# Kernel optimization log

Hardware: AMD Instinct MI355X
Metric: run time of the kernel (lower is better)

Reference implementation:

```python
import jax, jax.numpy as jnp
import numpy as np

B, S, D, H, F = 4, 1024, 512, 8, 2048
EPS = 1e-6


def _layernorm(x, g, b):
    m = jnp.mean(x, axis=-1, keepdims=True)
    v = jnp.mean(jnp.square(x - m), axis=-1, keepdims=True)
    return (x - m) * jax.lax.rsqrt(v + EPS) * g + b


def setup_inputs() -> dict:
    key = jax.random.key(0)
    ks = jax.random.split(key, 16)
    sd = 0.02
    return {
        "input_tensor": jax.random.normal(ks[0], (B, S, D), jnp.float32),
        # per-head QKV projections: each head maps D -> D (full depth, as in source)
        "Wq": jax.random.normal(ks[1], (H, D, D), jnp.float32) * sd,
        "bq": jnp.zeros((H, D), jnp.float32),
        "Wk": jax.random.normal(ks[2], (H, D, D), jnp.float32) * sd,
        "bk": jnp.zeros((H, D), jnp.float32),
        "Wv": jax.random.normal(ks[3], (H, D, D), jnp.float32) * sd,
        "bv": jnp.zeros((H, D), jnp.float32),
        # output projection after concat of H full-depth heads: (H*D) -> D
        "Wo": jax.random.normal(ks[4], (H * D, D), jnp.float32) * sd,
        "bo": jnp.zeros((D,), jnp.float32),
        "g1": jnp.ones((D,), jnp.float32),
        "beta1": jnp.zeros((D,), jnp.float32),
        "W1": jax.random.normal(ks[5], (D, F), jnp.float32) * sd,
        "b1": jnp.zeros((F,), jnp.float32),
        "W2": jax.random.normal(ks[6], (F, D), jnp.float32) * sd,
        "b2": jnp.zeros((D,), jnp.float32),
        "g2": jnp.ones((D,), jnp.float32),
        "beta2": jnp.zeros((D,), jnp.float32),
    }


def reference(input_tensor, Wq, bq, Wk, bk, Wv, bv, Wo, bo,
              g1, beta1, W1, b1, W2, b2, g2, beta2):
    x = input_tensor
    # batched per-head projections: [B,S,D] x [H,D,E] -> [B,H,S,E]
    q = jnp.einsum("bsd,hde->bhse", x, Wq) + bq[None, :, None, :]
    k = jnp.einsum("bsd,hde->bhse", x, Wk) + bk[None, :, None, :]
    v = jnp.einsum("bsd,hde->bhse", x, Wv) + bv[None, :, None, :]
    scale = 1.0 / jnp.sqrt(jnp.asarray(D, x.dtype))
    scores = jnp.einsum("bhse,bhte->bhst", q, k) * scale  # [B,H,S,S]
    attn = jax.nn.softmax(scores, axis=-1)
    heads = jnp.einsum("bhst,bhte->bhse", attn, v)  # [B,H,S,E]
    # concat heads on last axis: [B,S,H*D]
    concat = jnp.transpose(heads, (0, 2, 1, 3)).reshape(B, S, H * D)
    mha = concat @ Wo + bo  # [B,S,D]
    # dropout is identity at inference
    y = _layernorm(x + mha, g1, beta1)
    ff = jax.nn.relu(y @ W1 + b1) @ W2 + b2
    return _layernorm(y + ff, g2, beta2)
```

## Files before the change

### kernel.cpp

```cpp
#include <hip/hip_runtime.h>
#include <hip/hip_bf16.h>

typedef unsigned short u16;
typedef unsigned char u8;
typedef unsigned int u32;
typedef long long i64;
typedef __attribute__((ext_vector_type(4))) float f32x4;
typedef __attribute__((ext_vector_type(8))) __bf16 bf16x8;

#define DEV __device__ __forceinline__

DEV u16 f2bf(float f) {
  union { float f; unsigned u; } c; c.f = f;
  unsigned r = (c.u + 0x7fffu + ((c.u >> 16) & 1u)) >> 16;
  return (u16)r;
}

DEV float bf2f(u16 u) {
  union { u32 u; float f; } c; c.u = (u32)u << 16;
  return c.f;
}

DEV void gld_lds16(const void* g, void* l) {
  __builtin_amdgcn_global_load_lds(
      (__attribute__((address_space(1))) void*)g,
      (__attribute__((address_space(3))) void*)l, 16, 0, 0);
}

DEV f32x4 mfma_bf16(bf16x8 a, bf16x8 b, f32x4 c) {
  return __builtin_amdgcn_mfma_f32_16x16x32_bf16(a, b, c, 0, 0, 0);
}

DEV void bar_vm0() { asm volatile("s_waitcnt vmcnt(0) lgkmcnt(0)\n\ts_barrier" ::: "memory"); }
DEV void wait_lg0() { asm volatile("s_waitcnt lgkmcnt(0)" ::: "memory"); }

DEV u32 pack_fp8x4(float a, float b, float c, float d) {
  u32 t = __builtin_amdgcn_cvt_pk_fp8_f32(a, b, 0, false);
  t = __builtin_amdgcn_cvt_pk_fp8_f32(c, d, t, true);
  return t;
}

DEV u8 f2fp8(float v) {
  u32 t = __builtin_amdgcn_cvt_pk_fp8_f32(v, v, 0, false);
  return (u8)(t & 0xff);
}

__global__ __launch_bounds__(256) void prep_kernel(const float* __restrict__ x,
                                                   const float* __restrict__ Wq,
                                                   const float* __restrict__ Wk,
                                                   const float* __restrict__ Wv,
                                                   const float* __restrict__ Wo,
                                                   const float* __restrict__ W1,
                                                   const float* __restrict__ W2,
                                                   u16* __restrict__ xb, u16* __restrict__ wqC,
                                                   u16* __restrict__ wkC, u16* __restrict__ wvC,
                                                   u16* __restrict__ woT, u16* __restrict__ w1T,
                                                   u16* __restrict__ w2T) {
  int b = blockIdx.x;
  int tid = threadIdx.x;
  if (b < 8192) {
    const float* in;
    u16* out;
    int i;
    if (b < 2048) { in = x; out = xb; i = b * 256 + tid; }
    else {
      int idx = b - 2048;
      int job = idx >> 11;
      in = job == 0 ? Wq : (job == 1 ? Wk : Wv);
      out = job == 0 ? wqC : (job == 1 ? wkC : wvC);
      i = (idx & 2047) * 256 + tid;
    }
    float4 v = ((const float4*)in)[i];
    ushort4 o;
    o.x = f2bf(v.x); o.y = f2bf(v.y); o.z = f2bf(v.z); o.w = f2bf(v.w);
    ((ushort4*)out)[i] = o;
    return;
  }
  int idx = b - 8192;
  const float* in;
  u16* out;
  int R, C, bx, by;
  if (idx < 2048) { in = Wo; out = woT; R = 4096; C = 512; by = idx >> 4; bx = idx & 15; }
  else if (idx < 3072) { int rr = idx - 2048; in = W1; out = w1T; R = 512; C = 2048; by = rr >> 6; bx = rr & 63; }
  else { int rr = idx - 3072; in = W2; out = w2T; R = 2048; C = 512; by = rr >> 4; bx = rr & 15; }
  __shared__ float t[32][33];
  int c0 = bx * 32, r0 = by * 32;
  int tx = tid & 31, ty = tid >> 5;
#pragma unroll
  for (int i = 0; i < 4; ++i) {
    int rr2 = ty + i * 8;
    t[rr2][tx] = in[(size_t)(r0 + rr2) * C + c0 + tx];
  }
  __syncthreads();
#pragma unroll
  for (int i = 0; i < 4; ++i) {
    int cc = ty + i * 8;
    out[(size_t)(c0 + cc) * R + r0 + tx] = f2bf(t[tx][cc]);
  }
}

__global__ __launch_bounds__(256) void biasp_kernel(const float* __restrict__ Wo,
                                                    const float* __restrict__ bv,
                                                    float* __restrict__ biasP) {
  int b = blockIdx.x;
  int h = b >> 2, ec = b & 3;
  int t = threadIdx.x;
  int tl = t & 127, half = t >> 7;
  int e = ec * 128 + tl;
  float acc = 0.f;
  for (int i = 0; i < 256; ++i) {
    int e2 = half * 256 + i;
    acc += Wo[(size_t)(h * 512 + e2) * 512 + e] * bv[h * 512 + e2];
  }
  __shared__ float sh[2][128];
  sh[half][tl] = acc;
  __syncthreads();
  if (half == 0) biasP[h * 512 + e] = sh[0][tl] + sh[1][tl];
}

template <int AMODE>
__global__ __launch_bounds__(256) void gemm_bat(const u16* __restrict__ A,
                                                const u16* __restrict__ B,
                                                u16* __restrict__ out) {
  constexpr int BK = 64, BM = 128, BN = 128;
  __shared__ u16 As[2][BM * BK];
  __shared__ u16 Bs[2][BN * BK];
  const int tid = threadIdx.x;
  const int wave = tid >> 6, lane = tid & 63;
  const int r = lane & 15, g = lane >> 4;
  const int row0 = blockIdx.y * BM, col0 = blockIdx.x * BN;
  const int head = row0 >> 9;
  const int wr = (wave >> 1) * 64, wc = (wave & 1) * 64;

  auto stage = [&](int kt, int p) {
#pragma unroll
    for (int i = 0; i < 4; ++i) {
      int bi = i * 256 + wave * 64;
      int c = bi + lane;
      int row = c >> 3, ch = (c & 7) ^ (row & 7);
      size_t aoff;
      if constexpr (AMODE == 0)
        aoff = (size_t)(row0 + row) * 512 + kt + ch * 8;
      else
        aoff = (size_t)((row0 + row) & 511) * 4096 + head * 512 + kt + ch * 8;
      gld_lds16(A + aoff, &As[p][(size_t)bi * 8]);
    }
#pragma unroll
    for (int i = 0; i < 4; ++i) {
      int bi = i * 256 + wave * 64;
      int c = bi + lane;
      int row = c >> 3, ch = (c & 7) ^ (row & 7);
      gld_lds16(B + (size_t)(head * 512 + col0 + row) * 512 + kt + ch * 8,
                &Bs[p][(size_t)bi * 8]);
    }
  };

  f32x4 acc[4][4] = {};
  stage(0, 0);
  for (int t = 0; t < 8; ++t) {
    const int p = t & 1;
    bar_vm0();
    if (t < 7) stage((t + 1) * BK, p ^ 1);
    __builtin_amdgcn_s_setprio(1);
#pragma unroll
    for (int kk = 0; kk < 2; ++kk) {
      bf16x8 af[4], bfv[4];
#pragma unroll
      for (int m = 0; m < 4; ++m)
        af[m] = *(const bf16x8*)(&As[p][(wr + m * 16 + r) * BK + (((kk * 4 + g) ^ (r & 7))) * 8]);
#pragma unroll
      for (int n = 0; n < 4; ++n)
        bfv[n] = *(const bf16x8*)(&Bs[p][(wc + n * 16 + r) * BK + (((kk * 4 + g) ^ (r & 7))) * 8]);
#pragma unroll
      for (int m = 0; m < 4; ++m)
#pragma unroll
        for (int n = 0; n < 4; ++n)
          acc[m][n] = mfma_bf16(af[m], bfv[n], acc[m][n]);
    }
    __builtin_amdgcn_s_setprio(0);
  }
#pragma unroll
  for (int m = 0; m < 4; ++m)
#pragma unroll
    for (int n = 0; n < 4; ++n)
#pragma unroll
      for (int j = 0; j < 4; ++j)
        out[(size_t)(row0 + wr + m * 16 + g * 4 + j) * 512 + col0 + wc + n * 16 + r] =
            f2bf(acc[m][n][j]);
}

template <int NT, int BM, int BN, int WM, int WN, int MODE, int SPLITK>
__global__ __launch_bounds__(NT) void gemm_tn(const u16* __restrict__ A,
                                              const u16* __restrict__ B, int N, int K,
                                              void* __restrict__ out0,
                                              const float* __restrict__ bias0) {
  constexpr int BK = 64;
  constexpr int MF = WM / 16, NF = WN / 16;
  constexpr int WC = BN / WN;
  constexpr int AI = (BM * BK / 8) / NT;
  constexpr int BI = (BN * BK / 8) / NT;
  __shared__ u16 As[2][BM * BK];
  __shared__ u16 Bs[2][BN * BK];
  const int tid = threadIdx.x;
  const int wave = tid >> 6, lane = tid & 63;
  const int r = lane & 15, g = lane >> 4;
  const int row0 = blockIdx.y * BM, col0 = blockIdx.x * BN;
  const int wr = (wave / WC) * WM, wc = (wave % WC) * WN;
  const int KS = K * SPLITK;
  const int kb0 = blockIdx.z * K;

  auto stage = [&](int kt, int p) {
#pragma unroll
    for (int i = 0; i < AI; ++i) {
      int bi = i * NT + wave * 64;
      int c = bi + lane;
      int row = c >> 3, ch = (c & 7) ^ (row & 7);
      gld_lds16(A + (size_t)(row0 + row) * KS + kb0 + kt + ch * 8, &As[p][(size_t)bi * 8]);
    }
#pragma unroll
    for (int i = 0; i < BI; ++i) {
      int bi = i * NT + wave * 64;
      int c = bi + lane;
      int row = c >> 3, ch = (c & 7) ^ (row & 7);
      gld_lds16(B + (size_t)(col0 + row) * KS + kb0 + kt + ch * 8, &Bs[p][(size_t)bi * 8]);
    }
  };

  f32x4 acc[MF][NF] = {};
  const int nt = K / BK;

  stage(0, 0);
  for (int t = 0; t < nt; ++t) {
    const int p = t & 1;
    bar_vm0();
    if (t + 1 < nt) stage((t + 1) * BK, p ^ 1);
    __builtin_amdgcn_s_setprio(1);
#pragma unroll
    for (int kk = 0; kk < 2; ++kk) {
      bf16x8 af[MF], bfv[NF];
#pragma unroll
      for (int m = 0; m < MF; ++m)
        af[m] = *(const bf16x8*)(&As[p][(wr + m * 16 + r) * BK + (((kk * 4 + g) ^ (r & 7))) * 8]);
#pragma unroll
      for (int n = 0; n < NF; ++n)
        bfv[n] = *(const bf16x8*)(&Bs[p][(wc + n * 16 + r) * BK + (((kk * 4 + g) ^ (r & 7))) * 8]);
#pragma unroll
      for (int m = 0; m < MF; ++m)
#pragma unroll
        for (int n = 0; n < NF; ++n)
          acc[m][n] = mfma_bf16(af[m], bfv[n], acc[m][n]);
    }
    __builtin_amdgcn_s_setprio(0);
  }

  const size_t moff = (size_t)blockIdx.z * gridDim.y * BM * N;
#pragma unroll
  for (int m = 0; m < MF; ++m) {
#pragma unroll
    for (int n = 0; n < NF; ++n) {
      int gcol = col0 + wc + n * 16 + r;
#pragma unroll
      for (int j = 0; j < 4; ++j) {
        int grow = row0 + wr + m * 16 + g * 4 + j;
        float val = acc[m][n][j];
        if constexpr (MODE == 0) {
          int he = gcol;
          val += bias0[he];
          int bb = grow >> 10, s = grow & 1023;
          size_t off = (((size_t)(bb * 8 + (he >> 9)) * 1024 + s) * 512) + (he & 511);
          ((u16*)out0)[off] = f2bf(val);
        } else if constexpr (MODE == 1) {
          val += bias0[grow];
          int bb = gcol >> 10, s = gcol & 1023;
          size_t off = (((size_t)bb * 8 + (grow >> 9)) * 512 + (grow & 511)) * 1024 + s;
          ((u8*)out0)[off] = f2fp8(val);
        } else if constexpr (MODE == 2) {
          if (SPLITK == 1 || blockIdx.z == 0) val += bias0[gcol];
          ((float*)out0)[moff + (size_t)grow * N + gcol] = val;
        } else {
          float v2 = fmaxf(val + bias0[gcol], 0.0f);
          ((u16*)out0)[(size_t)grow * N + gcol] = f2bf(v2);
        }
      }
    }
  }
}

__global__ __launch_bounds__(512, 2) void flash_kernel(const u16* __restrict__ qg,
                                                       const u16* __restrict__ kg,
                                                       const u8* __restrict__ vtg,
                                                       u16* __restrict__ concat) {
  constexpr float SCALE = 0.04419417382415922f;
  __shared__ u16 Ks[2][32 * 512];
  __shared__ __align__(16) u8 VsB[2][16 * 1024];
  __shared__ __align__(16) u32 PsP[8][128];

  const int tid = threadIdx.x;
  const int wave = tid >> 6, lane = tid & 63;
  const int r = lane & 15, g = lane >> 4;
  const int bx = blockIdx.x;
  const int xcd = bx & 7, slot = bx >> 3;
  const int bh = xcd * 4 + (slot >> 3);
  const int qt = slot & 7;
  const int bb = bh >> 3, hh = bh & 7;
  const size_t hbase = (size_t)bh * 1024 * 512;
  const u16* qp = qg + hbase;
  const u16* kp = kg + (size_t)bb * 1024 * 512;
  const u8* vp = vtg + (size_t)bh * 512 * 1024;
  const int q0 = qt * 128;

  bf16x8 q[16];
#pragma unroll
  for (int kk = 0; kk < 16; ++kk)
    q[kk] = *(const bf16x8*)(qp + (size_t)(q0 + wave * 16 + r) * 512 + kk * 32 + g * 8);

  const int krow8 = lane >> 3, kch = (lane & 7) ^ (lane >> 3);
  const int vrow_s = lane >> 1;
  const int vsw_s = (vrow_s & 2) ^ ((vrow_s >> 2) & 2);
  const int vhalf = lane & 1;
  auto stageKV = [&](int t, int p) {
    int kv = t * 32;
#pragma unroll
    for (int j = 0; j < 4; ++j) {
      int id = wave * 4 + j;
      gld_lds16(kp + (size_t)(kv + j * 8 + krow8) * 512 + wave * 64 + kch * 8,
                &Ks[p][id * 512]);
    }
#pragma unroll
    for (int jj = 0; jj < 2; ++jj) {
      int nv = wave * 2 + jj;
      gld_lds16(vp + (size_t)(nv * 32 + vrow_s) * 1024 + kv + (((vhalf * 2) ^ vsw_s) * 8),
                &VsB[p][nv * 1024]);
    }
  };

  f32x4 o[32] = {};
  float mrun = -1e30f, lrun = 0.f;

  stageKV(0, 0);

  const int krh = (r >> 3) * 512;
  const int ke0 = (r & 7) * 64 + ((g ^ (r & 7)) * 8);
  const int ke1 = (r & 7) * 64 + (((4 + g) ^ (r & 7)) * 8);
  const int vsw = (r & 2) ^ ((r >> 2) & 2);
  const int vo8 = ((g ^ vsw) << 3);
  const int psw = r & 6;

  for (int t = 0; t < 32; ++t) {
    const int p = t & 1;
    bar_vm0();
    if (t < 31) stageKV(t + 1, p ^ 1);

    __builtin_amdgcn_s_setprio(1);
    f32x4 a0 = {}, a1 = {}, b0 = {}, b1 = {};
#pragma unroll
    for (int kc = 0; kc < 8; ++kc) {
      const u16* kb = &Ks[p][kc * 2048 + krh];
      bf16x8 kf00 = *(const bf16x8*)(kb + ke0);
      bf16x8 kf01 = *(const bf16x8*)(kb + 1024 + ke0);
      bf16x8 kf10 = *(const bf16x8*)(kb + ke1);
      bf16x8 kf11 = *(const bf16x8*)(kb + 1024 + ke1);
      a0 = mfma_bf16(kf00, q[2 * kc], a0);
      b0 = mfma_bf16(kf01, q[2 * kc], b0);
      a1 = mfma_bf16(kf10, q[2 * kc + 1], a1);
      b1 = mfma_bf16(kf11, q[2 * kc + 1], b1);
    }
    __builtin_amdgcn_s_setprio(0);
    f32x4 s0 = a0 + a1;
    f32x4 s1 = b0 + b1;

    float m8 = -1e30f;
#pragma unroll
    for (int j = 0; j < 4; ++j) {
      s0[j] *= SCALE;
      s1[j] *= SCALE;
      m8 = fmaxf(m8, fmaxf(s0[j], s1[j]));
    }
    m8 = fmaxf(m8, __shfl_xor(m8, 16));
    m8 = fmaxf(m8, __shfl_xor(m8, 32));
    if (__any(m8 - mrun > 6.0f)) {
      float mn = fmaxf(mrun, m8);
      float rs = __expf(mrun - mn);
      mrun = mn;
      lrun *= rs;
#pragma unroll
      for (int j = 0; j < 4; ++j) {
        float rsj = __shfl(rs, (lane & 48) | (g * 4 + j));
#pragma unroll
        for (int n = 0; n < 32; ++n) o[n][j] *= rsj;
      }
    }
    f32x4 p0, p1;
    float ls = 0.f;
#pragma unroll
    for (int j = 0; j < 4; ++j) {
      p0[j] = __expf(s0[j] - mrun);
      p1[j] = __expf(s1[j] - mrun);
      ls += p0[j] + p1[j];
    }
    ls += __shfl_xor(ls, 16);
    ls += __shfl_xor(ls, 32);
    lrun += ls;

    {
      u32* pw = PsP[wave];
      u32 wA = pack_fp8x4(p0[0], p0[1], p0[2], p0[3]);
      u32 wB = pack_fp8x4(p1[0], p1[1], p1[2], p1[3]);
      pw[r * 8 + (g ^ psw)] = wA;
      pw[r * 8 + ((4 + g) ^ psw)] = wB;
    }
    wait_lg0();

    i64 pa = *(const i64*)&PsP[wave][r * 8 + ((2 * g) ^ psw)];
    __builtin_amdgcn_s_setprio(1);
#pragma unroll
    for (int n = 0; n < 32; ++n) {
      int vrow = ((n & 1) << 4) + r;
      i64 bv = *(const i64*)&VsB[p][((n >> 1) << 10) + vrow * 32 + vo8];
      o[n] = __builtin_amdgcn_mfma_f32_16x16x32_fp8_fp8(pa, bv, o[n], 0, 0, 0);
    }
    __builtin_amdgcn_s_setprio(0);
  }

  float invl = 1.0f / lrun;
#pragma unroll
  for (int j = 0; j < 4; ++j) {
    float inv = __shfl(invl, (lane & 48) | (g * 4 + j));
    int srow = q0 + wave * 16 + g * 4 + j;
    size_t rowoff = ((size_t)bb * 1024 + srow) * 4096;
#pragma unroll
    for (int n = 0; n < 32; ++n) {
      int ocol = hh * 512 + n * 16 + r;
      concat[rowoff + ocol] = f2bf(o[n][j] * inv);
    }
  }
}

__global__ __launch_bounds__(128) void add_ln_kernel(const float* __restrict__ xin,
                                                     const u16* __restrict__ cc8,
                                                     const float* __restrict__ addin,
                                                     const float* __restrict__ addin2,
                                                     const float* __restrict__ bias,
                                                     const float* __restrict__ gamma,
                                                     const float* __restrict__ beta,
                                                     float* __restrict__ yout,
                                                     u16* __restrict__ ybout) {
  int row = blockIdx.x;
  int t = threadIdx.x;
  float4 xv = ((const float4*)(xin + (size_t)row * 512))[t];
  float v0 = xv.x, v1 = xv.y, v2 = xv.z, v3 = xv.w;
  if (cc8) {
    const u16* cr = cc8 + (size_t)row * 4096 + t * 4;
#pragma unroll
    for (int h = 0; h < 8; ++h) {
      ushort4 u = *(const ushort4*)(cr + h * 512);
      v0 += bf2f(u.x); v1 += bf2f(u.y); v2 += bf2f(u.z); v3 += bf2f(u.w);
    }
  }
  if (addin) {
    float4 av = ((const float4*)(addin + (size_t)row * 512))[t];
    v0 += av.x; v1 += av.y; v2 += av.z; v3 += av.w;
  }
  if (addin2) {
    float4 bv2 = ((const float4*)(addin2 + (size_t)row * 512))[t];
    v0 += bv2.x; v1 += bv2.y; v2 += bv2.z; v3 += bv2.w;
  }
  if (bias) {
    float4 b4 = ((const float4*)bias)[t];
    v0 += b4.x; v1 += b4.y; v2 += b4.z; v3 += b4.w;
  }
  float s1 = v0 + v1 + v2 + v3;
  float s2 = v0 * v0 + v1 * v1 + v2 * v2 + v3 * v3;
#pragma unroll
  for (int d = 1; d < 64; d <<= 1) {
    s1 += __shfl_xor(s1, d);
    s2 += __shfl_xor(s2, d);
  }
  __shared__ float sh[4];
  int wv = t >> 6;
  if ((t & 63) == 0) { sh[wv * 2] = s1; sh[wv * 2 + 1] = s2; }
  __syncthreads();
  s1 = sh[0] + sh[2];
  s2 = sh[1] + sh[3];
  float mean = s1 * (1.0f / 512.0f);
  float var = s2 * (1.0f / 512.0f) - mean * mean;
  float rstd = rsqrtf(var + 1e-6f);
  float4 gv = ((const float4*)gamma)[t];
  float4 bv = ((const float4*)beta)[t];
  float o0 = (v0 - mean) * rstd * gv.x + bv.x;
  float o1 = (v1 - mean) * rstd * gv.y + bv.y;
  float o2 = (v2 - mean) * rstd * gv.z + bv.z;
  float o3 = (v3 - mean) * rstd * gv.w + bv.w;
  float4 ov; ov.x = o0; ov.y = o1; ov.z = o2; ov.w = o3;
  ((float4*)(yout + (size_t)row * 512))[t] = ov;
  if (ybout) {
    ushort4 ub;
    ub.x = f2bf(o0); ub.y = f2bf(o1); ub.z = f2bf(o2); ub.w = f2bf(o3);
    ((ushort4*)(ybout + (size_t)row * 512))[t] = ub;
  }
}

extern "C" void kernel_launch(void* const* d_in, const int* in_sizes, int n_in, void* d_out,
                              int out_size, void* d_ws, size_t ws_size, hipStream_t stream) {
  (void)in_sizes; (void)n_in; (void)out_size; (void)ws_size;
  const float* x   = (const float*)d_in[0];
  const float* Wq  = (const float*)d_in[1];
  const float* bq  = (const float*)d_in[2];
  const float* Wk  = (const float*)d_in[3];
  const float* bk  = (const float*)d_in[4];
  const float* Wv  = (const float*)d_in[5];
  const float* bv  = (const float*)d_in[6];
  const float* Wo  = (const float*)d_in[7];
  const float* bo  = (const float*)d_in[8];
  const float* g1  = (const float*)d_in[9];
  const float* be1 = (const float*)d_in[10];
  const float* W1  = (const float*)d_in[11];
  const float* b1  = (const float*)d_in[12];
  const float* W2  = (const float*)d_in[13];
  const float* b2  = (const float*)d_in[14];
  const float* g2  = (const float*)d_in[15];
  const float* be2 = (const float*)d_in[16];
  (void)bk;

  char* ws = (char*)d_ws;
  const size_t MB = 1024 * 1024;
  u16*   xb    = (u16*)(ws + 0);
  u16*   wqC   = (u16*)(ws + 4 * MB);
  u16*   wkC   = (u16*)(ws + 8 * MB);
  u16*   wvC   = (u16*)(ws + 12 * MB);
  u16*   woT   = (u16*)(ws + 16 * MB);
  u16*   w1T   = (u16*)(ws + 20 * MB);
  u16*   w2T   = (u16*)(ws + 22 * MB);
  float* biasP = (float*)(ws + 24 * MB);
  u16*   mhT   = (u16*)(ws + 26 * MB);
  u16*   nhT   = (u16*)(ws + 30 * MB);
  u16*   qb    = (u16*)(ws + 34 * MB);
  u8*    vTb   = (u8*)(ws + 66 * MB);
  u16*   cc    = (u16*)(ws + 98 * MB);
  float* y     = (float*)(ws + 4 * MB);
  u16*   yb    = (u16*)(ws + 26 * MB);
  u16*   ff1   = (u16*)(ws + 34 * MB);
  float* ff2a  = (float*)(ws + 50 * MB);
  float* ff2b  = (float*)(ws + 58 * MB);

  prep_kernel<<<12288, 256, 0, stream>>>(x, Wq, Wk, Wv, Wo, W1, W2, xb, wqC, wkC, wvC,
                                         woT, w1T, w2T);
  biasp_kernel<<<32, 256, 0, stream>>>(Wo, bv, biasP);
  gemm_bat<0><<<dim3(4, 32), 256, 0, stream>>>(wkC, wqC, mhT);
  gemm_bat<1><<<dim3(4, 32), 256, 0, stream>>>(woT, wvC, nhT);
  gemm_tn<512, 256, 256, 128, 64, 0, 1><<<dim3(16, 16), 512, 0, stream>>>(xb, mhT, 4096, 512, qb, bq);
  gemm_tn<512, 256, 256, 128, 64, 1, 1><<<dim3(16, 16), 512, 0, stream>>>(nhT, xb, 4096, 512, vTb, biasP);
  flash_kernel<<<256, 512, 0, stream>>>(qb, xb, vTb, cc);
  add_ln_kernel<<<4096, 128, 0, stream>>>(x, cc, nullptr, nullptr, bo, g1, be1, y, yb);
  gemm_tn<256, 128, 128, 64, 64, 3, 1><<<dim3(16, 32), 256, 0, stream>>>(yb, w1T, 2048, 512, ff1, b1);
  gemm_tn<256, 64, 128, 32, 64, 2, 2><<<dim3(4, 64, 2), 256, 0, stream>>>(ff1, w2T, 512, 1024, ff2a, b2);
  add_ln_kernel<<<4096, 128, 0, stream>>>(y, nullptr, ff2a, ff2b, nullptr, g2, be2, (float*)d_out, nullptr);
}
```

Measured before the change: 250.0 us.

## Load V fragments directly from global in MFMA-ready tiled layout, drop V LDS staging

The V-transpose projection epilogue now writes fp8 V in a tiled layout of 32-key blocks, [bh][s/32][e][s%32]. The flash kernel can then read each lane's 8-byte MFMA B-operand straight from global/L2 into registers instead of staging through LDS with global_load_lds. This removes the V LDS buffers and the LDS reads in the PV loop, freeing shared memory. The cost is per-lane 8-byte global loads issued inside the loop, with their latency only partly hidden behind the softmax work. V is also no longer shared across waves through LDS, so each wave fetches the whole V tile itself.

```diff
diff --git a/kernel.cpp b/kernel.cpp
--- a/kernel.cpp
+++ b/kernel.cpp
@@ -271,8 +271,10 @@
           ((u16*)out0)[off] = f2bf(val);
         } else if constexpr (MODE == 1) {
           val += bias0[grow];
-          int bb = gcol >> 10, s = gcol & 1023;
-          size_t off = (((size_t)bb * 8 + (grow >> 9)) * 512 + (grow & 511)) * 1024 + s;
+          int h = grow >> 9, e_ = grow & 511;
+          int bbb = gcol >> 10, s = gcol & 1023;
+          size_t off = ((size_t)(bbb * 8 + h)) * 524288 + (size_t)(s >> 5) * 16384 +
+                       (size_t)e_ * 32 + (s & 31);
           ((u8*)out0)[off] = f2fp8(val);
         } else if constexpr (MODE == 2) {
           if (SPLITK == 1 || blockIdx.z == 0) val += bias0[gcol];
@@ -292,7 +294,6 @@
                                                        u16* __restrict__ concat) {
   constexpr float SCALE = 0.04419417382415922f;
   __shared__ u16 Ks[2][32 * 512];
-  __shared__ __align__(16) u8 VsB[2][16 * 1024];
   __shared__ __align__(16) u32 PsP[8][128];
 
   const int tid = threadIdx.x;
@@ -306,7 +307,7 @@
   const size_t hbase = (size_t)bh * 1024 * 512;
   const u16* qp = qg + hbase;
   const u16* kp = kg + (size_t)bb * 1024 * 512;
-  const u8* vp = vtg + (size_t)bh * 512 * 1024;
+  const u8* vp = vtg + (size_t)bh * 524288;
   const int q0 = qt * 128;
 
   bf16x8 q[16];
@@ -315,10 +316,7 @@
     q[kk] = *(const bf16x8*)(qp + (size_t)(q0 + wave * 16 + r) * 512 + kk * 32 + g * 8);
 
   const int krow8 = lane >> 3, kch = (lane & 7) ^ (lane >> 3);
-  const int vrow_s = lane >> 1;
-  const int vsw_s = (vrow_s & 2) ^ ((vrow_s >> 2) & 2);
-  const int vhalf = lane & 1;
-  auto stageKV = [&](int t, int p) {
+  auto stageK = [&](int t, int p) {
     int kv = t * 32;
 #pragma unroll
     for (int j = 0; j < 4; ++j) {
@@ -326,30 +324,23 @@
       gld_lds16(kp + (size_t)(kv + j * 8 + krow8) * 512 + wave * 64 + kch * 8,
                 &Ks[p][id * 512]);
     }
-#pragma unroll
-    for (int jj = 0; jj < 2; ++jj) {
-      int nv = wave * 2 + jj;
-      gld_lds16(vp + (size_t)(nv * 32 + vrow_s) * 1024 + kv + (((vhalf * 2) ^ vsw_s) * 8),
-                &VsB[p][nv * 1024]);
-    }
   };
 
   f32x4 o[32] = {};
   float mrun = -1e30f, lrun = 0.f;
 
-  stageKV(0, 0);
+  stageK(0, 0);
 
   const int krh = (r >> 3) * 512;
   const int ke0 = (r & 7) * 64 + ((g ^ (r & 7)) * 8);
   const int ke1 = (r & 7) * 64 + (((4 + g) ^ (r & 7)) * 8);
-  const int vsw = (r & 2) ^ ((r >> 2) & 2);
-  const int vo8 = ((g ^ vsw) << 3);
+  const u8* vbl = vp + r * 32 + g * 8;
   const int psw = r & 6;
 
   for (int t = 0; t < 32; ++t) {
     const int p = t & 1;
     bar_vm0();
-    if (t < 31) stageKV(t + 1, p ^ 1);
+    if (t < 31) stageK(t + 1, p ^ 1);
 
     __builtin_amdgcn_s_setprio(1);
     f32x4 a0 = {}, a1 = {}, b0 = {}, b1 = {};
@@ -369,6 +360,11 @@
     f32x4 s0 = a0 + a1;
     f32x4 s1 = b0 + b1;
 
+    const u8* vb = vbl + (size_t)t * 16384;
+    i64 vr[16];
+#pragma unroll
+    for (int k = 0; k < 16; ++k) vr[k] = *(const i64*)(vb + k * 512);
+
     float m8 = -1e30f;
 #pragma unroll
     for (int j = 0; j < 4; ++j) {
@@ -414,11 +410,15 @@
     i64 pa = *(const i64*)&PsP[wave][r * 8 + ((2 * g) ^ psw)];
     __builtin_amdgcn_s_setprio(1);
 #pragma unroll
-    for (int n = 0; n < 32; ++n) {
-      int vrow = ((n & 1) << 4) + r;
-      i64 bv = *(const i64*)&VsB[p][((n >> 1) << 10) + vrow * 32 + vo8];
-      o[n] = __builtin_amdgcn_mfma_f32_16x16x32_fp8_fp8(pa, bv, o[n], 0, 0, 0);
-    }
+    for (int n = 0; n < 16; ++n)
+      o[n] = __builtin_amdgcn_mfma_f32_16x16x32_fp8_fp8(pa, vr[n], o[n], 0, 0, 0);
+    __builtin_amdgcn_s_setprio(0);
+#pragma unroll
+    for (int k = 0; k < 16; ++k) vr[k] = *(const i64*)(vb + 8192 + k * 512);
+    __builtin_amdgcn_s_setprio(1);
+#pragma unroll
+    for (int n = 0; n < 16; ++n)
+      o[16 + n] = __builtin_amdgcn_mfma_f32_16x16x32_fp8_fp8(pa, vr[n], o[16 + n], 0, 0, 0);
     __builtin_amdgcn_s_setprio(0);
   }
 
```

Measured after the change: 432.3 us. 1.73x slower.
